# Performance work log

Measured on AMD Instinct MI355X. Metric: run time of the kernel, lower is better.

The kernel has to match this reference:

```python
import jax, jax.numpy as jnp
import numpy as np

B, S, I, C = 1, 2048, 384, 64
H, CH = 8, 8  # n_head, c_h
EPS_LN = 1e-5


def setup_inputs() -> dict:
    key = jax.random.key(0)
    ks = jax.random.split(key, 8)
    sc = lambda fan_in: 1.0 / np.sqrt(fan_in)
    return {
        "m": jax.random.normal(ks[0], (B, S, I, C), dtype=jnp.float32),
        "mask": jnp.ones((B, S, I), dtype=jnp.float32),
        "ln_gamma": jnp.ones((C,), dtype=jnp.float32),
        "ln_beta": jnp.zeros((C,), dtype=jnp.float32),
        "Wq": jax.random.normal(ks[1], (H * CH, C), dtype=jnp.float32) * sc(C),
        "Wk": jax.random.normal(ks[2], (CH, C), dtype=jnp.float32) * sc(C),
        "Wv": jax.random.normal(ks[3], (CH, C), dtype=jnp.float32) * sc(C),
        "Wg": jax.random.normal(ks[4], (H * CH, C), dtype=jnp.float32) * sc(C),
        "bg": jnp.zeros((H * CH,), dtype=jnp.float32),
        "Wo": jax.random.normal(ks[5], (C, H * CH), dtype=jnp.float32) * sc(H * CH),
        "bo": jnp.zeros((C,), dtype=jnp.float32),
    }


def _layernorm(x, gamma, beta):
    mu = x.mean(axis=-1, keepdims=True)
    var = x.var(axis=-1, keepdims=True)
    return (x - mu) * jax.lax.rsqrt(var + EPS_LN) * gamma + beta


def reference(m, mask, ln_gamma, ln_beta, Wq, Wk, Wv, Wg, bg, Wo, bo):
    # m: [B, s, i, c]; mask: [B, s, i]
    m_col = jnp.swapaxes(m, -2, -3)          # [B, i, s, c]
    mask_col = jnp.swapaxes(mask, -1, -2)    # [B, i, s]
    m_norm = _layernorm(m_col, ln_gamma, ln_beta)

    # masked-mean global query per column
    denom = jnp.clip(mask_col.sum(axis=-1, keepdims=True), 1e-5, None)  # [B, i, 1]
    q_global = (m_norm * mask_col[..., None]).sum(axis=-2) / denom      # [B, i, c]

    q = (q_global @ Wq.T).reshape(*q_global.shape[:-1], H, CH)  # [B, i, H, CH]
    k = m_norm @ Wk.T                                           # [B, i, s, CH]
    v = m_norm @ Wv.T                                           # [B, i, s, CH]

    scale = 1.0 / np.sqrt(CH)
    logits = jnp.einsum("bihc,bisc->bihs", q, k) * scale        # [B, i, H, s]
    logits = jnp.where(mask_col[:, :, None, :] > 0, logits, -1e9)
    attn = jax.nn.softmax(logits, axis=-1)
    ctx = jnp.einsum("bihs,bisc->bihc", attn, v)                # [B, i, H, CH]

    g = jax.nn.sigmoid(m_norm @ Wg.T + bg)                      # [B, i, s, H*CH]
    o = ctx.reshape(*ctx.shape[:-2], 1, H * CH) * g             # [B, i, s, H*CH]
    out = o @ Wo.T + bo                                          # [B, i, s, c]
    return jnp.swapaxes(out, -2, -3)                             # [B, s, i, c]
```

## Files before the change

kernel.cpp:

```cpp
#include <hip/hip_runtime.h>

#define IDIM 384
#define SDIM 2048
#define NCH  8
#define CHUNK 256

#define WS_STATS 0
#define WS_QGP   (IDIM*SDIM*2)
#define WS_Q     (WS_QGP + IDIM*NCH*65)
#define WS_ATT   (WS_Q + IDIM*64)
#define WS_CTX   (WS_ATT + IDIM*NCH*8*10)
#define WS_WGT   (WS_CTX + IDIM*64)
#define WS_WOT   (WS_WGT + 64*64)

typedef float f16v __attribute__((ext_vector_type(16)));

__global__ __launch_bounds__(64) void kW(const float* __restrict__ Wg,
                                         const float* __restrict__ Wo,
                                         float* __restrict__ ws) {
    int a = blockIdx.x, t = threadIdx.x;
    ws[WS_WGT + a * 64 + t] = Wg[t * 64 + a];
    ws[WS_WOT + a * 64 + t] = Wo[t * 64 + a];
}

__global__ __launch_bounds__(256) void kA(const float* __restrict__ m,
                                          const float* __restrict__ mask,
                                          const float* __restrict__ gamma,
                                          const float* __restrict__ beta,
                                          float* __restrict__ ws) {
    int bx = blockIdx.x;
    int i = bx >> 3, chk = bx & 7;
    int tid = threadIdx.x;
    int rg = tid >> 3;
    int c8 = tid & 7;
    float4 ga4 = *(const float4*)&gamma[c8 * 8];
    float4 gb4 = *(const float4*)&gamma[c8 * 8 + 4];
    float4 ba4 = *(const float4*)&beta[c8 * 8];
    float4 bb4 = *(const float4*)&beta[c8 * 8 + 4];
    float g[8] = {ga4.x, ga4.y, ga4.z, ga4.w, gb4.x, gb4.y, gb4.z, gb4.w};
    float b[8] = {ba4.x, ba4.y, ba4.z, ba4.w, bb4.x, bb4.y, bb4.z, bb4.w};
    float qg[8];
    #pragma unroll
    for (int j = 0; j < 8; ++j) qg[j] = 0.f;
    float cnt = 0.f;
    float* stats = ws + WS_STATS;

    for (int t = 0; t < 8; ++t) {
        int s = chk * CHUNK + t * 32 + rg;
        const float* mp = &m[((size_t)s * IDIM + i) * 64 + c8 * 8];
        float4 xa = *(const float4*)mp;
        float4 xb = *(const float4*)(mp + 4);
        float x[8] = {xa.x, xa.y, xa.z, xa.w, xb.x, xb.y, xb.z, xb.w};
        float sx = 0.f, sxx = 0.f;
        #pragma unroll
        for (int j = 0; j < 8; ++j) { sx += x[j]; sxx += x[j] * x[j]; }
        sx += __shfl_xor(sx, 1); sxx += __shfl_xor(sxx, 1);
        sx += __shfl_xor(sx, 2); sxx += __shfl_xor(sxx, 2);
        sx += __shfl_xor(sx, 4); sxx += __shfl_xor(sxx, 4);
        float mu  = sx * (1.f / 64.f);
        float var = sxx * (1.f / 64.f) - mu * mu;
        float rs  = rsqrtf(var + 1e-5f);
        float mk  = mask[s * IDIM + i];
        #pragma unroll
        for (int j = 0; j < 8; ++j) {
            float mn = (x[j] - mu) * rs * g[j] + b[j];
            qg[j] += mk * mn;
        }
        if (c8 == 0) {
            cnt += mk;
            float2 st = {mu, rs};
            *(float2*)&stats[((size_t)i * SDIM + s) * 2] = st;
        }
    }
    __shared__ float red[32][68];
    #pragma unroll
    for (int j = 0; j < 8; ++j) red[rg][c8 * 8 + j] = qg[j];
    if (c8 == 0) red[rg][64] = cnt;
    __syncthreads();
    if (tid < 65) {
        float v = 0.f;
        #pragma unroll
        for (int r = 0; r < 32; ++r) v += red[r][tid];
        ws[WS_QGP + (i * NCH + chk) * 65 + tid] = v;
    }
}

__global__ __launch_bounds__(64) void kB(const float* __restrict__ Wq,
                                         float* __restrict__ ws) {
    int i = blockIdx.x, l = threadIdx.x;
    float sum = 0.f, cnt = 0.f;
    #pragma unroll
    for (int c = 0; c < NCH; ++c) {
        sum += ws[WS_QGP + (i * NCH + c) * 65 + l];
        cnt += ws[WS_QGP + (i * NCH + c) * 65 + 64];
    }
    float denom = fmaxf(cnt, 1e-5f);
    __shared__ float qg[64];
    qg[l] = sum / denom;
    __syncthreads();
    float acc = 0.f;
    #pragma unroll 8
    for (int c = 0; c < 64; ++c) acc += qg[c] * Wq[l * 64 + c];
    ws[WS_Q + i * 64 + l] = acc * 0.35355339059327373f;
}

__global__ __launch_bounds__(256) void kC(const float* __restrict__ m,
                                          const float* __restrict__ mask,
                                          const float* __restrict__ gamma,
                                          const float* __restrict__ beta,
                                          const float* __restrict__ Wk,
                                          const float* __restrict__ Wv,
                                          float* __restrict__ ws) {
    int bx = blockIdx.x;
    int i = bx >> 3, chk = bx & 7;
    int tid = threadIdx.x;
    __shared__ float mnT[32 * 68];
    __shared__ float Wk_s[8 * 68], Wv_s[8 * 68];
    __shared__ float k_s[32 * 9], v_s[32 * 9];
    __shared__ float q_s[64];
    __shared__ float red[32 * 8 * 10];
    const float* stats = ws + WS_STATS;

    if (tid < 64) q_s[tid] = ws[WS_Q + i * 64 + tid];
    for (int idx = tid; idx < 512; idx += 256) {
        int r = idx >> 6, c = idx & 63;
        Wk_s[r * 68 + c] = Wk[idx];
        Wv_s[r * 68 + c] = Wv[idx];
    }

    int sr = tid >> 3;
    int lo = tid & 7;
    float m_run = -1e30f, l_run = 0.f, ctx[8];
    #pragma unroll
    for (int z = 0; z < 8; ++z) ctx[z] = 0.f;
    __syncthreads();

    for (int t = 0; t < 8; ++t) {
        int sbase = chk * CHUNK + t * 32;
        for (int idx = tid; idx < 512; idx += 256) {
            int r = idx >> 4, c4 = idx & 15;
            int s = sbase + r;
            float4 x4 = *(const float4*)&m[((size_t)s * IDIM + i) * 64 + c4 * 4];
            float4 g4 = *(const float4*)&gamma[c4 * 4];
            float4 b4 = *(const float4*)&beta[c4 * 4];
            float2 st = *(const float2*)&stats[((size_t)i * SDIM + s) * 2];
            float4 mn;
            mn.x = (x4.x - st.x) * st.y * g4.x + b4.x;
            mn.y = (x4.y - st.x) * st.y * g4.y + b4.y;
            mn.z = (x4.z - st.x) * st.y * g4.z + b4.z;
            mn.w = (x4.w - st.x) * st.y * g4.w + b4.w;
            *(float4*)&mnT[r * 68 + c4 * 4] = mn;
        }
        __syncthreads();
        {
            float accK = 0.f, accV = 0.f;
            #pragma unroll
            for (int c4 = 0; c4 < 16; ++c4) {
                float4 a  = *(const float4*)&mnT[sr * 68 + c4 * 4];
                float4 wk = *(const float4*)&Wk_s[lo * 68 + c4 * 4];
                float4 wv = *(const float4*)&Wv_s[lo * 68 + c4 * 4];
                accK += a.x * wk.x + a.y * wk.y + a.z * wk.z + a.w * wk.w;
                accV += a.x * wv.x + a.y * wv.y + a.z * wv.z + a.w * wv.w;
            }
            k_s[sr * 9 + lo] = accK;
            v_s[sr * 9 + lo] = accV;
        }
        __syncthreads();
        {
            float lg = 0.f;
            #pragma unroll
            for (int c = 0; c < 8; ++c) lg += q_s[lo * 8 + c] * k_s[sr * 9 + c];
            float mk = mask[(sbase + sr) * IDIM + i];
            lg = (mk > 0.f) ? lg : -1e9f;
            float mnew = fmaxf(m_run, lg);
            float al = expf(m_run - mnew);
            float p  = expf(lg - mnew);
            l_run = l_run * al + p;
            #pragma unroll
            for (int c = 0; c < 8; ++c) ctx[c] = ctx[c] * al + p * v_s[sr * 9 + c];
            m_run = mnew;
        }
        __syncthreads();
    }
    int base = (sr * 8 + lo) * 10;
    red[base] = m_run; red[base + 1] = l_run;
    #pragma unroll
    for (int c = 0; c < 8; ++c) red[base + 2 + c] = ctx[c];
    __syncthreads();
    if (tid < 8) {
        int h = tid;
        float M = -1e30f;
        for (int r = 0; r < 32; ++r) M = fmaxf(M, red[(r * 8 + h) * 10]);
        float L = 0.f, CT[8];
        #pragma unroll
        for (int c = 0; c < 8; ++c) CT[c] = 0.f;
        for (int r = 0; r < 32; ++r) {
            float e = expf(red[(r * 8 + h) * 10] - M);
            L += red[(r * 8 + h) * 10 + 1] * e;
            for (int c = 0; c < 8; ++c) CT[c] += red[(r * 8 + h) * 10 + 2 + c] * e;
        }
        float* dst = ws + WS_ATT + ((i * NCH + chk) * 8 + h) * 10;
        dst[0] = M; dst[1] = L;
        for (int c = 0; c < 8; ++c) dst[2 + c] = CT[c];
    }
}

__global__ __launch_bounds__(64) void kD(float* __restrict__ ws) {
    int i = blockIdx.x, l = threadIdx.x;
    int h = l >> 3, c2 = l & 7;
    float M = -1e30f;
    #pragma unroll
    for (int c = 0; c < NCH; ++c)
        M = fmaxf(M, ws[WS_ATT + ((i * NCH + c) * 8 + h) * 10]);
    float L = 0.f, CT = 0.f;
    #pragma unroll
    for (int c = 0; c < NCH; ++c) {
        const float* src = ws + WS_ATT + ((i * NCH + c) * 8 + h) * 10;
        float e = expf(src[0] - M);
        L += src[1] * e;
        CT += src[2 + c2] * e;
    }
    ws[WS_CTX + i * 64 + l] = CT / L;
}

__global__ __launch_bounds__(256, 4) void kE(const float* __restrict__ m,
                                             const float* __restrict__ gamma,
                                             const float* __restrict__ beta,
                                             const float* __restrict__ bg,
                                             const float* __restrict__ bo,
                                             const float* __restrict__ ws,
                                             float* __restrict__ out) {
    int bx = blockIdx.x;
    int i = bx >> 4;
    int tile = bx & 15;
    int tid = threadIdx.x;
    int l = tid & 63;
    int wv16 = __builtin_amdgcn_readfirstlane((tid >> 6) << 4);
    __shared__ float mnT[128 * 68];
    const float* stats = ws + WS_STATS;
    int s0 = tile * 128;

    float ctxv[16], bgv[16], bov[16];
    #pragma unroll
    for (int q = 0; q < 4; ++q) {
        float4 cv = *(const float4*)&ws[WS_CTX + i * 64 + wv16 + q * 4];
        float4 gv = *(const float4*)&bg[wv16 + q * 4];
        float4 ov = *(const float4*)&bo[wv16 + q * 4];
        ctxv[q*4+0]=cv.x; ctxv[q*4+1]=cv.y; ctxv[q*4+2]=cv.z; ctxv[q*4+3]=cv.w;
        bgv[q*4+0]=gv.x;  bgv[q*4+1]=gv.y;  bgv[q*4+2]=gv.z;  bgv[q*4+3]=gv.w;
        bov[q*4+0]=ov.x;  bov[q*4+1]=ov.y;  bov[q*4+2]=ov.z;  bov[q*4+3]=ov.w;
    }

    for (int idx = tid; idx < 2048; idx += 256) {
        int r = idx >> 4, c4 = idx & 15;
        int s = s0 + r;
        float4 x4 = *(const float4*)&m[((size_t)s * IDIM + i) * 64 + c4 * 4];
        float4 g4 = *(const float4*)&gamma[c4 * 4];
        float4 b4 = *(const float4*)&beta[c4 * 4];
        float2 st = *(const float2*)&stats[((size_t)i * SDIM + s) * 2];
        float4 mn;
        mn.x = (x4.x - st.x) * st.y * g4.x + b4.x;
        mn.y = (x4.y - st.x) * st.y * g4.y + b4.y;
        mn.z = (x4.z - st.x) * st.y * g4.z + b4.z;
        mn.w = (x4.w - st.x) * st.y * g4.w + b4.w;
        *(float4*)&mnT[r * 68 + c4 * 4] = mn;
    }
    __syncthreads();

    float z0[16], z1[16];
    #pragma unroll
    for (int jj = 0; jj < 16; ++jj) { z0[jj] = 0.f; z1[jj] = 0.f; }
    const float* aP0 = &mnT[l * 68];
    const float* aP1 = &mnT[(l + 64) * 68];

    {
        const float* Bg = ws + WS_WGT + wv16;
        #pragma unroll 4
        for (int c4 = 0; c4 < 16; ++c4) {
            float4 a0 = *(const float4*)(aP0 + c4 * 4);
            float4 a1 = *(const float4*)(aP1 + c4 * 4);
            float a0a[4] = {a0.x, a0.y, a0.z, a0.w};
            float a1a[4] = {a1.x, a1.y, a1.z, a1.w};
            #pragma unroll
            for (int cc = 0; cc < 4; ++cc) {
                f16v bv = *(const f16v*)(Bg + (c4 * 4 + cc) * 64);
                float av0 = a0a[cc], av1 = a1a[cc];
                #pragma unroll
                for (int jj = 0; jj < 16; ++jj) {
                    z0[jj] += av0 * bv[jj];
                    z1[jj] += av1 * bv[jj];
                }
            }
        }
    }
    __syncthreads();

    #pragma unroll
    for (int jj = 0; jj < 16; ++jj) {
        z0[jj] = ctxv[jj] / (1.f + expf(-(z0[jj] + bgv[jj])));
        z1[jj] = ctxv[jj] / (1.f + expf(-(z1[jj] + bgv[jj])));
    }
    #pragma unroll
    for (int q = 0; q < 4; ++q) {
        float4 t0 = {z0[q*4+0], z0[q*4+1], z0[q*4+2], z0[q*4+3]};
        float4 t1 = {z1[q*4+0], z1[q*4+1], z1[q*4+2], z1[q*4+3]};
        *(float4*)&mnT[l * 68 + wv16 + q * 4]        = t0;
        *(float4*)&mnT[(l + 64) * 68 + wv16 + q * 4] = t1;
    }
    #pragma unroll
    for (int jj = 0; jj < 16; ++jj) { z0[jj] = 0.f; z1[jj] = 0.f; }
    __syncthreads();

    {
        const float* Bo = ws + WS_WOT + wv16;
        #pragma unroll 4
        for (int c4 = 0; c4 < 16; ++c4) {
            float4 a0 = *(const float4*)(aP0 + c4 * 4);
            float4 a1 = *(const float4*)(aP1 + c4 * 4);
            float a0a[4] = {a0.x, a0.y, a0.z, a0.w};
            float a1a[4] = {a1.x, a1.y, a1.z, a1.w};
            #pragma unroll
            for (int cc = 0; cc < 4; ++cc) {
                f16v bv = *(const f16v*)(Bo + (c4 * 4 + cc) * 64);
                float av0 = a0a[cc], av1 = a1a[cc];
                #pragma unroll
                for (int jj = 0; jj < 16; ++jj) {
                    z0[jj] += av0 * bv[jj];
                    z1[jj] += av1 * bv[jj];
                }
            }
        }
    }
    __syncthreads();

    #pragma unroll
    for (int q = 0; q < 4; ++q) {
        float4 t0 = {z0[q*4+0]+bov[q*4+0], z0[q*4+1]+bov[q*4+1],
                     z0[q*4+2]+bov[q*4+2], z0[q*4+3]+bov[q*4+3]};
        float4 t1 = {z1[q*4+0]+bov[q*4+0], z1[q*4+1]+bov[q*4+1],
                     z1[q*4+2]+bov[q*4+2], z1[q*4+3]+bov[q*4+3]};
        *(float4*)&mnT[l * 68 + wv16 + q * 4]        = t0;
        *(float4*)&mnT[(l + 64) * 68 + wv16 + q * 4] = t1;
    }
    __syncthreads();

    for (int idx = tid; idx < 2048; idx += 256) {
        int r = idx >> 4, c4 = idx & 15;
        float4 v = *(const float4*)&mnT[r * 68 + c4 * 4];
        *(float4*)&out[((size_t)(s0 + r) * IDIM + i) * 64 + c4 * 4] = v;
    }
}

extern "C" void kernel_launch(void* const* d_in, const int* in_sizes, int n_in,
                              void* d_out, int out_size, void* d_ws, size_t ws_size,
                              hipStream_t stream) {
    const float* m    = (const float*)d_in[0];
    const float* mask = (const float*)d_in[1];
    const float* gam  = (const float*)d_in[2];
    const float* bet  = (const float*)d_in[3];
    const float* Wq   = (const float*)d_in[4];
    const float* Wk   = (const float*)d_in[5];
    const float* Wv   = (const float*)d_in[6];
    const float* Wg   = (const float*)d_in[7];
    const float* bg   = (const float*)d_in[8];
    const float* Wo   = (const float*)d_in[9];
    const float* bo   = (const float*)d_in[10];
    float* out = (float*)d_out;
    float* ws  = (float*)d_ws;
    (void)in_sizes; (void)n_in; (void)out_size; (void)ws_size;

    kW<<<64, 64, 0, stream>>>(Wg, Wo, ws);
    kA<<<IDIM * NCH, 256, 0, stream>>>(m, mask, gam, bet, ws);
    kB<<<IDIM, 64, 0, stream>>>(Wq, ws);
    kC<<<IDIM * NCH, 256, 0, stream>>>(m, mask, gam, bet, Wk, Wv, ws);
    kD<<<IDIM, 64, 0, stream>>>(ws);
    kE<<<IDIM * (SDIM / 128), 256, 0, stream>>>(m, gam, bet, bg, bo, ws, out);
}
```

Measured before the change: 615.7 us.

## Compute K/V projections in stats pass, drop second m read, retile output kernel

The first pass over m now also projects the normalized rows onto Wk and Wv and stores a compact 16-float K/V record per (i,s) in workspace. A new attention kernel reads only those records, so the second full read of m is gone. The weight transpose kernel is folded into kB, and kE is retiled to 64 rows per block with higher occupancy bounds. The fused path needs a larger workspace and falls back to the old path when the workspace is too small, which makes it unclear whether it runs by default.

Measured after the change: 602.8 us. 1.02x faster.

```diff
diff --git a/kernel.cpp b/kernel.cpp
--- a/kernel.cpp
+++ b/kernel.cpp
@@ -12,27 +12,32 @@
 #define WS_CTX   (WS_ATT + IDIM*NCH*8*10)
 #define WS_WGT   (WS_CTX + IDIM*64)
 #define WS_WOT   (WS_WGT + 64*64)
+#define WS_KV    (WS_WOT + 64*64)
 
 typedef float f16v __attribute__((ext_vector_type(16)));
 
-__global__ __launch_bounds__(64) void kW(const float* __restrict__ Wg,
-                                         const float* __restrict__ Wo,
-                                         float* __restrict__ ws) {
-    int a = blockIdx.x, t = threadIdx.x;
-    ws[WS_WGT + a * 64 + t] = Wg[t * 64 + a];
-    ws[WS_WOT + a * 64 + t] = Wo[t * 64 + a];
-}
-
-__global__ __launch_bounds__(256) void kA(const float* __restrict__ m,
-                                          const float* __restrict__ mask,
-                                          const float* __restrict__ gamma,
-                                          const float* __restrict__ beta,
-                                          float* __restrict__ ws) {
+template<bool DOKV>
+__global__ __launch_bounds__(256) void kA2(const float* __restrict__ m,
+                                           const float* __restrict__ mask,
+                                           const float* __restrict__ gamma,
+                                           const float* __restrict__ beta,
+                                           const float* __restrict__ Wk,
+                                           const float* __restrict__ Wv,
+                                           float* __restrict__ ws) {
     int bx = blockIdx.x;
     int i = bx >> 3, chk = bx & 7;
     int tid = threadIdx.x;
     int rg = tid >> 3;
     int c8 = tid & 7;
+    __shared__ float Wk_s[8 * 68], Wv_s[8 * 68];
+    if (DOKV) {
+        for (int idx = tid; idx < 512; idx += 256) {
+            int r = idx >> 6, c = idx & 63;
+            Wk_s[r * 68 + c] = Wk[idx];
+            Wv_s[r * 68 + c] = Wv[idx];
+        }
+        __syncthreads();
+    }
     float4 ga4 = *(const float4*)&gamma[c8 * 8];
     float4 gb4 = *(const float4*)&gamma[c8 * 8 + 4];
     float4 ba4 = *(const float4*)&beta[c8 * 8];
@@ -61,15 +66,41 @@
         float var = sxx * (1.f / 64.f) - mu * mu;
         float rs  = rsqrtf(var + 1e-5f);
         float mk  = mask[s * IDIM + i];
+        float mnv[8];
         #pragma unroll
         for (int j = 0; j < 8; ++j) {
-            float mn = (x[j] - mu) * rs * g[j] + b[j];
-            qg[j] += mk * mn;
+            mnv[j] = (x[j] - mu) * rs * g[j] + b[j];
+            qg[j] += mk * mnv[j];
         }
         if (c8 == 0) {
             cnt += mk;
             float2 st = {mu, rs};
             *(float2*)&stats[((size_t)i * SDIM + s) * 2] = st;
+        }
+        if (DOKV) {
+            float kp[8], vp[8];
+            #pragma unroll
+            for (int h = 0; h < 8; ++h) {
+                float4 wk0 = *(const float4*)&Wk_s[h * 68 + c8 * 8];
+                float4 wk1 = *(const float4*)&Wk_s[h * 68 + c8 * 8 + 4];
+                float4 wv0 = *(const float4*)&Wv_s[h * 68 + c8 * 8];
+                float4 wv1 = *(const float4*)&Wv_s[h * 68 + c8 * 8 + 4];
+                kp[h] = mnv[0]*wk0.x + mnv[1]*wk0.y + mnv[2]*wk0.z + mnv[3]*wk0.w
+                      + mnv[4]*wk1.x + mnv[5]*wk1.y + mnv[6]*wk1.z + mnv[7]*wk1.w;
+                vp[h] = mnv[0]*wv0.x + mnv[1]*wv0.y + mnv[2]*wv0.z + mnv[3]*wv0.w
+                      + mnv[4]*wv1.x + mnv[5]*wv1.y + mnv[6]*wv1.z + mnv[7]*wv1.w;
+            }
+            #pragma unroll
+            for (int h = 0; h < 8; ++h) {
+                kp[h] += __shfl_xor(kp[h], 1); vp[h] += __shfl_xor(vp[h], 1);
+                kp[h] += __shfl_xor(kp[h], 2); vp[h] += __shfl_xor(vp[h], 2);
+                kp[h] += __shfl_xor(kp[h], 4); vp[h] += __shfl_xor(vp[h], 4);
+            }
+            float* kvp = ws + WS_KV + ((size_t)i * SDIM + s) * 16;
+            #pragma unroll
+            for (int j = 0; j < 8; ++j) {
+                if (c8 == j) { kvp[j] = kp[j]; kvp[8 + j] = vp[j]; }
+            }
         }
     }
     __shared__ float red[32][68];
@@ -86,8 +117,14 @@
 }
 
 __global__ __launch_bounds__(64) void kB(const float* __restrict__ Wq,
+                                         const float* __restrict__ Wg,
+                                         const float* __restrict__ Wo,
                                          float* __restrict__ ws) {
     int i = blockIdx.x, l = threadIdx.x;
+    if (i < 64) {
+        ws[WS_WGT + i * 64 + l] = Wg[l * 64 + i];
+        ws[WS_WOT + i * 64 + l] = Wo[l * 64 + i];
+    }
     float sum = 0.f, cnt = 0.f;
     #pragma unroll
     for (int c = 0; c < NCH; ++c) {
@@ -102,6 +139,70 @@
     #pragma unroll 8
     for (int c = 0; c < 64; ++c) acc += qg[c] * Wq[l * 64 + c];
     ws[WS_Q + i * 64 + l] = acc * 0.35355339059327373f;
+}
+
+__global__ __launch_bounds__(256) void kC2(const float* __restrict__ mask,
+                                           float* __restrict__ ws) {
+    int bx = blockIdx.x;
+    int i = bx >> 3, chk = bx & 7;
+    int tid = threadIdx.x;
+    __shared__ float kv_s[256 * 20];
+    __shared__ float red[32 * 8 * 10];
+
+    const float* kvg = ws + WS_KV + ((size_t)i * SDIM + chk * CHUNK) * 16;
+    for (int idx = tid; idx < 1024; idx += 256) {
+        int r = idx >> 2, c4 = idx & 3;
+        *(float4*)&kv_s[r * 20 + c4 * 4] = *(const float4*)&kvg[idx * 4];
+    }
+    int sr = tid >> 3;
+    int lo = tid & 7;
+    const float* wq = ws + WS_Q + i * 64 + lo * 8;
+    float4 q0 = *(const float4*)wq;
+    float4 q1 = *(const float4*)(wq + 4);
+    float m_run = -1e30f, l_run = 0.f, ctx[8];
+    #pragma unroll
+    for (int z = 0; z < 8; ++z) ctx[z] = 0.f;
+    __syncthreads();
+
+    for (int t = 0; t < 8; ++t) {
+        int r = t * 32 + sr;
+        float4 k0 = *(const float4*)&kv_s[r * 20];
+        float4 k1 = *(const float4*)&kv_s[r * 20 + 4];
+        float4 v0 = *(const float4*)&kv_s[r * 20 + 8];
+        float4 v1 = *(const float4*)&kv_s[r * 20 + 12];
+        float lg = q0.x*k0.x + q0.y*k0.y + q0.z*k0.z + q0.w*k0.w
+                 + q1.x*k1.x + q1.y*k1.y + q1.z*k1.z + q1.w*k1.w;
+        float mk = mask[(chk * CHUNK + r) * IDIM + i];
+        lg = (mk > 0.f) ? lg : -1e9f;
+        float mnew = fmaxf(m_run, lg);
+        float al = expf(m_run - mnew);
+        float p  = expf(lg - mnew);
+        l_run = l_run * al + p;
+        ctx[0] = ctx[0]*al + p*v0.x; ctx[1] = ctx[1]*al + p*v0.y;
+        ctx[2] = ctx[2]*al + p*v0.z; ctx[3] = ctx[3]*al + p*v0.w;
+        ctx[4] = ctx[4]*al + p*v1.x; ctx[5] = ctx[5]*al + p*v1.y;
+        ctx[6] = ctx[6]*al + p*v1.z; ctx[7] = ctx[7]*al + p*v1.w;
+        m_run = mnew;
+    }
+    int base = (sr * 8 + lo) * 10;
+    red[base] = m_run; red[base + 1] = l_run;
+    #pragma unroll
+    for (int c = 0; c < 8; ++c) red[base + 2 + c] = ctx[c];
+    __syncthreads();
+    if (tid < 64) {
+        int h = tid >> 3, c2 = tid & 7;
+        float M = -1e30f;
+        for (int r = 0; r < 32; ++r) M = fmaxf(M, red[(r * 8 + h) * 10]);
+        float L = 0.f, CT = 0.f;
+        for (int r = 0; r < 32; ++r) {
+            float e = expf(red[(r * 8 + h) * 10] - M);
+            L += red[(r * 8 + h) * 10 + 1] * e;
+            CT += red[(r * 8 + h) * 10 + 2 + c2] * e;
+        }
+        float* dst = ws + WS_ATT + ((i * NCH + chk) * 8 + h) * 10;
+        if (c2 == 0) { dst[0] = M; dst[1] = L; }
+        dst[2 + c2] = CT;
+    }
 }
 
 __global__ __launch_bounds__(256) void kC(const float* __restrict__ m,
@@ -127,7 +228,6 @@
         Wk_s[r * 68 + c] = Wk[idx];
         Wv_s[r * 68 + c] = Wv[idx];
     }
-
     int sr = tid >> 3;
     int lo = tid & 7;
     float m_run = -1e30f, l_run = 0.f, ctx[8];
@@ -187,21 +287,19 @@
     #pragma unroll
     for (int c = 0; c < 8; ++c) red[base + 2 + c] = ctx[c];
     __syncthreads();
-    if (tid < 8) {
-        int h = tid;
+    if (tid < 64) {
+        int h = tid >> 3, c2 = tid & 7;
         float M = -1e30f;
         for (int r = 0; r < 32; ++r) M = fmaxf(M, red[(r * 8 + h) * 10]);
-        float L = 0.f, CT[8];
-        #pragma unroll
-        for (int c = 0; c < 8; ++c) CT[c] = 0.f;
+        float L = 0.f, CT = 0.f;
         for (int r = 0; r < 32; ++r) {
             float e = expf(red[(r * 8 + h) * 10] - M);
             L += red[(r * 8 + h) * 10 + 1] * e;
-            for (int c = 0; c < 8; ++c) CT[c] += red[(r * 8 + h) * 10 + 2 + c] * e;
+            CT += red[(r * 8 + h) * 10 + 2 + c2] * e;
         }
         float* dst = ws + WS_ATT + ((i * NCH + chk) * 8 + h) * 10;
-        dst[0] = M; dst[1] = L;
-        for (int c = 0; c < 8; ++c) dst[2 + c] = CT[c];
+        if (c2 == 0) { dst[0] = M; dst[1] = L; }
+        dst[2 + c2] = CT;
     }
 }
 
@@ -223,7 +321,7 @@
     ws[WS_CTX + i * 64 + l] = CT / L;
 }
 
-__global__ __launch_bounds__(256, 4) void kE(const float* __restrict__ m,
+__global__ __launch_bounds__(256, 8) void kE(const float* __restrict__ m,
                                              const float* __restrict__ gamma,
                                              const float* __restrict__ beta,
                                              const float* __restrict__ bg,
@@ -231,14 +329,14 @@
                                              const float* __restrict__ ws,
                                              float* __restrict__ out) {
     int bx = blockIdx.x;
-    int i = bx >> 4;
-    int tile = bx & 15;
+    int i = bx >> 5;
+    int tile = bx & 31;
     int tid = threadIdx.x;
     int l = tid & 63;
     int wv16 = __builtin_amdgcn_readfirstlane((tid >> 6) << 4);
-    __shared__ float mnT[128 * 68];
+    __shared__ float mnT[64 * 68];
     const float* stats = ws + WS_STATS;
-    int s0 = tile * 128;
+    int s0 = tile * 64;
 
     float ctxv[16], bgv[16], bov[16];
     #pragma unroll
@@ -251,7 +349,7 @@
         bov[q*4+0]=ov.x;  bov[q*4+1]=ov.y;  bov[q*4+2]=ov.z;  bov[q*4+3]=ov.w;
     }
 
-    for (int idx = tid; idx < 2048; idx += 256) {
+    for (int idx = tid; idx < 1024; idx += 256) {
         int r = idx >> 4, c4 = idx & 15;
         int s = s0 + r;
         float4 x4 = *(const float4*)&m[((size_t)s * IDIM + i) * 64 + c4 * 4];
@@ -267,67 +365,52 @@
     }
     __syncthreads();
 
-    float z0[16], z1[16];
-    #pragma unroll
-    for (int jj = 0; jj < 16; ++jj) { z0[jj] = 0.f; z1[jj] = 0.f; }
-    const float* aP0 = &mnT[l * 68];
-    const float* aP1 = &mnT[(l + 64) * 68];
+    float z[16];
+    #pragma unroll
+    for (int jj = 0; jj < 16; ++jj) z[jj] = 0.f;
+    const float* aP = &mnT[l * 68];
 
     {
         const float* Bg = ws + WS_WGT + wv16;
         #pragma unroll 4
         for (int c4 = 0; c4 < 16; ++c4) {
-            float4 a0 = *(const float4*)(aP0 + c4 * 4);
-            float4 a1 = *(const float4*)(aP1 + c4 * 4);
-            float a0a[4] = {a0.x, a0.y, a0.z, a0.w};
-            float a1a[4] = {a1.x, a1.y, a1.z, a1.w};
+            float4 a0 = *(const float4*)(aP + c4 * 4);
+            float aa[4] = {a0.x, a0.y, a0.z, a0.w};
             #pragma unroll
             for (int cc = 0; cc < 4; ++cc) {
                 f16v bv = *(const f16v*)(Bg + (c4 * 4 + cc) * 64);
-                float av0 = a0a[cc], av1 = a1a[cc];
+                float av = aa[cc];
                 #pragma unroll
-                for (int jj = 0; jj < 16; ++jj) {
-                    z0[jj] += av0 * bv[jj];
-                    z1[jj] += av1 * bv[jj];
-                }
-            }
-        }
-    }
-    __syncthreads();
-
-    #pragma unroll
-    for (int jj = 0; jj < 16; ++jj) {
-        z0[jj] = ctxv[jj] / (1.f + expf(-(z0[jj] + bgv[jj])));
-        z1[jj] = ctxv[jj] / (1.f + expf(-(z1[jj] + bgv[jj])));
-    }
+                for (int jj = 0; jj < 16; ++jj) z[jj] += av * bv[jj];
+            }
+        }
+    }
+    __syncthreads();
+
+    #pragma unroll
+    for (int jj = 0; jj < 16; ++jj)
+        z[jj] = ctxv[jj] / (1.f + expf(-(z[jj] + bgv[jj])));
     #pragma unroll
     for (int q = 0; q < 4; ++q) {
-        float4 t0 = {z0[q*4+0], z0[q*4+1], z0[q*4+2], z0[q*4+3]};
-        float4 t1 = {z1[q*4+0], z1[q*4+1], z1[q*4+2], z1[q*4+3]};
-        *(float4*)&mnT[l * 68 + wv16 + q * 4]        = t0;
-        *(float4*)&mnT[(l + 64) * 68 + wv16 + q * 4] = t1;
-    }
-    #pragma unroll
-    for (int jj = 0; jj < 16; ++jj) { z0[jj] = 0.f; z1[jj] = 0.f; }
+        float4 t0 = {z[q*4+0], z[q*4+1], z[q*4+2], z[q*4+3]};
+        *(float4*)&mnT[l * 68 + wv16 + q * 4] = t0;
+    }
+    #pragma unroll
+    for (int jj = 0; jj < 16; ++jj) z[jj] = 0.f;
     __syncthreads();
 
     {
         const float* Bo = ws + WS_WOT + wv16;
         #pragma unroll 4
         for (int c4 = 0; c4 < 16; ++c4) {
-            float4 a0 = *(const float4*)(aP0 + c4 * 4);
-            float4 a1 = *(const float4*)(aP1 + c4 * 4);
-            float a0a[4] = {a0.x, a0.y, a0.z, a0.w};
-            float a1a[4] = {a1.x, a1.y, a1.z, a1.w};
+            float4 a0 = *(const float4*)(aP + c4 * 4);
+            float aa[4] = {a0.x, a0.y, a0.z, a0.w};
             #pragma unroll
             for (int cc = 0; cc < 4; ++cc) {
                 f16v bv = *(const f16v*)(Bo + (c4 * 4 + cc) * 64);
-                float av0 = a0a[cc], av1 = a1a[cc];
+                float av = aa[cc];
                 #pragma unroll
-                for (int jj = 0; jj < 16; ++jj) {
-                    z0[jj] += av0 * bv[jj];
-                    z1[jj] += av1 * bv[jj];
-                }
+                for (int jj = 0; jj < 16; ++jj) z[jj] += av * bv[jj];
             }
         }
     }
@@ -335,16 +418,13 @@
 
     #pragma unroll
     for (int q = 0; q < 4; ++q) {
-        float4 t0 = {z0[q*4+0]+bov[q*4+0], z0[q*4+1]+bov[q*4+1],
-                     z0[q*4+2]+bov[q*4+2], z0[q*4+3]+bov[q*4+3]};
-        float4 t1 = {z1[q*4+0]+bov[q*4+0], z1[q*4+1]+bov[q*4+1],
-                     z1[q*4+2]+bov[q*4+2], z1[q*4+3]+bov[q*4+3]};
-        *(float4*)&mnT[l * 68 + wv16 + q * 4]        = t0;
-        *(float4*)&mnT[(l + 64) * 68 + wv16 + q * 4] = t1;
-    }
-    __syncthreads();
-
-    for (int idx = tid; idx < 2048; idx += 256) {
+        float4 t0 = {z[q*4+0]+bov[q*4+0], z[q*4+1]+bov[q*4+1],
+                     z[q*4+2]+bov[q*4+2], z[q*4+3]+bov[q*4+3]};
+        *(float4*)&mnT[l * 68 + wv16 + q * 4] = t0;
+    }
+    __syncthreads();
+
+    for (int idx = tid; idx < 1024; idx += 256) {
         int r = idx >> 4, c4 = idx & 15;
         float4 v = *(const float4*)&mnT[r * 68 + c4 * 4];
         *(float4*)&out[((size_t)(s0 + r) * IDIM + i) * 64 + c4 * 4] = v;
@@ -367,12 +447,20 @@
     const float* bo   = (const float*)d_in[10];
     float* out = (float*)d_out;
     float* ws  = (float*)d_ws;
-    (void)in_sizes; (void)n_in; (void)out_size; (void)ws_size;
-
-    kW<<<64, 64, 0, stream>>>(Wg, Wo, ws);
-    kA<<<IDIM * NCH, 256, 0, stream>>>(m, mask, gam, bet, ws);
-    kB<<<IDIM, 64, 0, stream>>>(Wq, ws);
-    kC<<<IDIM * NCH, 256, 0, stream>>>(m, mask, gam, bet, Wk, Wv, ws);
+    (void)in_sizes; (void)n_in; (void)out_size;
+
+    size_t need_fused = (size_t)(WS_KV + (size_t)IDIM * SDIM * 16) * sizeof(float);
+    bool fused = ws_size >= need_fused;
+
+    if (fused)
+        kA2<true><<<IDIM * NCH, 256, 0, stream>>>(m, mask, gam, bet, Wk, Wv, ws);
+    else
+        kA2<false><<<IDIM * NCH, 256, 0, stream>>>(m, mask, gam, bet, Wk, Wv, ws);
+    kB<<<IDIM, 64, 0, stream>>>(Wq, Wg, Wo, ws);
+    if (fused)
+        kC2<<<IDIM * NCH, 256, 0, stream>>>(mask, ws);
+    else
+        kC<<<IDIM * NCH, 256, 0, stream>>>(m, mask, gam, bet, Wk, Wv, ws);
     kD<<<IDIM, 64, 0, stream>>>(ws);
-    kE<<<IDIM * (SDIM / 128), 256, 0, stream>>>(m, gam, bet, bg, bo, ws, out);
-}
+    kE<<<IDIM * (SDIM / 64), 256, 0, stream>>>(m, gam, bet, bg, bo, ws, out);
+}
```
